# Optimization experiments

Measured on AMD Instinct MI355X. Metric: run time of the kernel, lower is better.

The kernel has to match this reference:

```python
import jax, jax.numpy as jnp
import numpy as np

N_NODES = 50000
N_EDGES = 600000
N_GRAPHS = 256


def gcn_conv(x, W, b, src, dst, n):
    # PyG GCNConv: out = D^{-1/2} (A + I) D^{-1/2} X W + b
    h = x @ W  # [N, out]
    deg = jax.ops.segment_sum(jnp.ones((src.shape[0],), h.dtype), dst, num_segments=n) + 1.0  # self-loop
    dinv = jax.lax.rsqrt(deg)  # deg >= 1 so safe
    msgs = h[src] * (dinv[src] * dinv[dst])[:, None]  # [E, out]
    agg = jax.ops.segment_sum(msgs, dst, num_segments=n)
    agg = agg + h * (dinv * dinv)[:, None]  # self-loop contribution
    return agg + b


def setup_inputs() -> dict:
    key = jax.random.key(0)
    ks = jax.random.split(key, 8)
    x = jax.random.normal(ks[0], (N_NODES, 1), dtype=jnp.float32)
    edge_index = jax.random.randint(ks[1], (2, N_EDGES), 0, N_NODES, dtype=jnp.int64)
    batch = jnp.sort(jax.random.randint(ks[2], (N_NODES,), 0, N_GRAPHS, dtype=jnp.int64))

    def glorot(k, shape):
        lim = np.sqrt(6.0 / (shape[0] + shape[1]))
        return jax.random.uniform(k, shape, jnp.float32, -lim, lim)

    return {
        "x": x,
        "W1": glorot(ks[3], (1, 64)), "b1": jnp.zeros((64,), jnp.float32),
        "W2": glorot(ks[4], (64, 128)), "b2": jnp.zeros((128,), jnp.float32),
        "W3": glorot(ks[5], (128, 64)), "b3": jnp.zeros((64,), jnp.float32),
        "lin1_w": glorot(ks[6], (64, 32)), "lin1_b": jnp.zeros((32,), jnp.float32),
        "lin2_w": glorot(ks[7], (32, 1)), "lin2_b": jnp.zeros((1,), jnp.float32),
        "edge_index": edge_index,
        "batch": batch,
    }


def reference(x, W1, b1, W2, b2, W3, b3, lin1_w, lin1_b, lin2_w, lin2_b, edge_index, batch):
    src, dst = edge_index[0], edge_index[1]
    n = x.shape[0]
    h = jax.nn.relu(gcn_conv(x, W1, b1, src, dst, n))
    h = jax.nn.relu(gcn_conv(h, W2, b2, src, dst, n))
    h = jax.nn.relu(gcn_conv(h, W3, b3, src, dst, n))
    # global_mean_pool
    sums = jax.ops.segment_sum(h, batch, num_segments=N_GRAPHS)
    cnts = jax.ops.segment_sum(jnp.ones((n,), h.dtype), batch, num_segments=N_GRAPHS)
    pooled = sums / jnp.maximum(cnts, 1.0)[:, None]  # [G, 64]
    z = jax.nn.relu(pooled @ lin1_w + lin1_b)
    return z @ lin2_w + lin2_b  # [G, 1]
```

## Files before the change

kernel.cpp:

```cpp
#include <hip/hip_runtime.h>


#define N_FEAT 64
#define POOL_SUB 16
#define SLOT 64

__global__ void fill_kernel(const int* __restrict__ src, const int* __restrict__ dst,
                            int* __restrict__ deg, int* __restrict__ csr, int E) {
    int e2 = (blockIdx.x * blockDim.x + threadIdx.x) * 2;
    if (e2 + 1 < E) {
        int2 sv = *(const int2*)&src[e2];
        int2 dv = *(const int2*)&dst[e2];
        int p0 = atomicAdd(&deg[dv.x], 1);
        int p1 = atomicAdd(&deg[dv.y], 1);
        csr[dv.x * SLOT + p0] = sv.x;
        csr[dv.y * SLOT + p1] = sv.y;
    } else if (e2 < E) {
        int d = dst[e2];
        int pos = atomicAdd(&deg[d], 1);
        csr[d * SLOT + pos] = src[e2];
    }
}

__global__ void prep_kernel(const int* __restrict__ deg, const float* __restrict__ x,
                            float* __restrict__ dinv, float* __restrict__ xd, int N) {
    int i = blockIdx.x * blockDim.x + threadIdx.x;
    if (i < N) {
        float dv = rsqrtf((float)deg[i] + 1.0f);
        dinv[i] = dv;
        xd[i] = x[i] * dv;
    }
}

__global__ void sagg_gather(const int* __restrict__ deg, const int* __restrict__ csr,
                            const float* __restrict__ xd, const float* __restrict__ dinv,
                            float2* __restrict__ sd, int N) {
    int wid = (blockIdx.x * blockDim.x + threadIdx.x) >> 6;
    int lane = threadIdx.x & 63;
    int v = wid * 4 + (lane >> 4);
    int sub = lane & 15;
    if (v >= N) return;
    int dg = deg[v];
    int base = v * SLOT;
    float sum = 0.0f;
    for (int j = sub; j < dg; j += 16) sum += xd[csr[base + j]];
    #pragma unroll
    for (int off = 8; off; off >>= 1) sum += __shfl_xor(sum, off);
    if (sub == 0) {
        float dv = dinv[v];
        sd[v] = make_float2(dv * (sum + xd[v]), dv);
    }
}

__global__ void agg1_gather(const int* __restrict__ deg, const int* __restrict__ csr,
                            const float2* __restrict__ sd,
                            const float* __restrict__ W1, const float* __restrict__ b1,
                            float* __restrict__ agg, int N) {
    int v = blockIdx.x * 4 + (threadIdx.x >> 6);
    int lane = threadIdx.x & 63;
    if (v >= N) return;
    float w1 = W1[lane], bb = b1[lane];
    int dg = deg[v];
    int base = v * SLOT;
    float acc = 0.0f;
    int j = 0;
    for (; j + 3 < dg; j += 4) {
        int u0 = csr[base + j], u1 = csr[base + j + 1];
        int u2 = csr[base + j + 2], u3 = csr[base + j + 3];
        float2 p0 = sd[u0];
        float2 p1 = sd[u1];
        float2 p2 = sd[u2];
        float2 p3 = sd[u3];
        acc += fmaxf(p0.x * w1 + bb, 0.0f) * p0.y + fmaxf(p1.x * w1 + bb, 0.0f) * p1.y;
        acc += fmaxf(p2.x * w1 + bb, 0.0f) * p2.y + fmaxf(p3.x * w1 + bb, 0.0f) * p3.y;
    }
    for (; j < dg; ++j) {
        float2 p = sd[csr[base + j]];
        acc += fmaxf(p.x * w1 + bb, 0.0f) * p.y;
    }
    float2 pv = sd[v];
    float dv = pv.y;
    agg[(size_t)v * N_FEAT + lane] = dv * acc + fmaxf(pv.x * w1 + bb, 0.0f) * dv * dv;
}

#define H2S 132
#define BM 32
__global__ __launch_bounds__(256) void gemm12(const float* __restrict__ A,
                                              const float* __restrict__ W2,
                                              const float* __restrict__ bias2,
                                              const float* __restrict__ W3,
                                              const float* __restrict__ dinv,
                                              float* __restrict__ md, int M) {
    __shared__ float Ws[128 * 64];
    __shared__ float Hs[BM * H2S];
    int tid = threadIdx.x;
    int row0 = blockIdx.x * BM;

    for (int idx = tid; idx < 64 * 128; idx += 256) Ws[idx] = W2[idx];
    {
        int r = tid >> 3;
        int kk = (tid & 7) * 8;
        int grow = row0 + r;
        float4 v0 = make_float4(0.f, 0.f, 0.f, 0.f), v1 = v0;
        if (grow < M) {
            v0 = *(const float4*)&A[(size_t)grow * 64 + kk];
            v1 = *(const float4*)&A[(size_t)grow * 64 + kk + 4];
        }
        *(float4*)&Hs[r * 64 + kk] = v0;
        *(float4*)&Hs[r * 64 + kk + 4] = v1;
    }
    __syncthreads();

    int c = (tid & 31) * 4;
    int rb = (tid >> 5) * 4;
    float acc1[4][4] = {};
    #pragma unroll 4
    for (int k = 0; k < 64; ++k) {
        float4 b = *(const float4*)&Ws[k * 128 + c];
        #pragma unroll
        for (int i = 0; i < 4; ++i) {
            float a = Hs[(rb + i) * 64 + k];
            acc1[i][0] += a * b.x; acc1[i][1] += a * b.y;
            acc1[i][2] += a * b.z; acc1[i][3] += a * b.w;
        }
    }
    float4 bv = *(const float4*)&bias2[c];
    __syncthreads();

    #pragma unroll
    for (int i = 0; i < 4; ++i) {
        float4 o;
        o.x = fmaxf(acc1[i][0] + bv.x, 0.f);
        o.y = fmaxf(acc1[i][1] + bv.y, 0.f);
        o.z = fmaxf(acc1[i][2] + bv.z, 0.f);
        o.w = fmaxf(acc1[i][3] + bv.w, 0.f);
        *(float4*)&Hs[(rb + i) * H2S + c] = o;
    }
    for (int idx = tid; idx < 128 * 64; idx += 256) Ws[idx] = W3[idx];
    __syncthreads();

    int c2 = (tid & 15) * 4;
    int r2 = (tid >> 4) * 2;
    float acc2[2][4] = {};
    for (int k0 = 0; k0 < 128; k0 += 4) {
        float4 w0 = *(const float4*)&Ws[(k0 + 0) * 64 + c2];
        float4 w1 = *(const float4*)&Ws[(k0 + 1) * 64 + c2];
        float4 w2 = *(const float4*)&Ws[(k0 + 2) * 64 + c2];
        float4 w3 = *(const float4*)&Ws[(k0 + 3) * 64 + c2];
        #pragma unroll
        for (int i = 0; i < 2; ++i) {
            float4 a = *(const float4*)&Hs[(r2 + i) * H2S + k0];
            acc2[i][0] += a.x * w0.x + a.y * w1.x + a.z * w2.x + a.w * w3.x;
            acc2[i][1] += a.x * w0.y + a.y * w1.y + a.z * w2.y + a.w * w3.y;
            acc2[i][2] += a.x * w0.z + a.y * w1.z + a.z * w2.z + a.w * w3.z;
            acc2[i][3] += a.x * w0.w + a.y * w1.w + a.z * w2.w + a.w * w3.w;
        }
    }
    #pragma unroll
    for (int i = 0; i < 2; ++i) {
        int grow = row0 + r2 + i;
        if (grow < M) {
            float dv = dinv[grow];
            float4 o = make_float4(acc2[i][0] * dv, acc2[i][1] * dv,
                                   acc2[i][2] * dv, acc2[i][3] * dv);
            *(float4*)&md[(size_t)grow * 64 + c2] = o;
        }
    }
}

__global__ void agg3_gather(const int* __restrict__ deg, const int* __restrict__ csr,
                            const float* __restrict__ md, const float* __restrict__ dinv,
                            float* __restrict__ agg, int N) {
    int v = blockIdx.x * 4 + (threadIdx.x >> 6);
    int lane = threadIdx.x & 63;
    if (v >= N) return;
    int dg = deg[v];
    int base = v * SLOT;
    float acc = md[(size_t)v * N_FEAT + lane];
    int j = 0;
    for (; j + 7 < dg; j += 8) {
        int u0 = csr[base + j],     u1 = csr[base + j + 1];
        int u2 = csr[base + j + 2], u3 = csr[base + j + 3];
        int u4 = csr[base + j + 4], u5 = csr[base + j + 5];
        int u6 = csr[base + j + 6], u7 = csr[base + j + 7];
        float a0 = md[(size_t)u0 * N_FEAT + lane];
        float a1 = md[(size_t)u1 * N_FEAT + lane];
        float a2 = md[(size_t)u2 * N_FEAT + lane];
        float a3 = md[(size_t)u3 * N_FEAT + lane];
        float a4 = md[(size_t)u4 * N_FEAT + lane];
        float a5 = md[(size_t)u5 * N_FEAT + lane];
        float a6 = md[(size_t)u6 * N_FEAT + lane];
        float a7 = md[(size_t)u7 * N_FEAT + lane];
        acc += ((a0 + a1) + (a2 + a3)) + ((a4 + a5) + (a6 + a7));
    }
    for (; j < dg; ++j) acc += md[(size_t)csr[base + j] * N_FEAT + lane];
    agg[(size_t)v * N_FEAT + lane] = acc * dinv[v];
}

__global__ void pool_kernel(const float* __restrict__ agg, const float* __restrict__ b3,
                            const int* __restrict__ batch, float* __restrict__ pooled,
                            float* __restrict__ counts, int N) {
    int wave = (blockIdx.x * blockDim.x + threadIdx.x) >> 6;
    int lane = threadIdx.x & 63;
    int start = wave * POOL_SUB;
    if (start >= N) return;
    int end = min(start + POOL_SUB, N);
    float bl = b3[lane];
    int cur = batch[start];
    float acc = 0.0f;
    float cnt = 0.0f;
    for (int i = start; i < end; ++i) {
        int g = batch[i];
        if (g != cur) {
            atomicAdd(&pooled[cur * N_FEAT + lane], acc);
            if (lane == 0) atomicAdd(&counts[cur], cnt);
            acc = 0.0f; cnt = 0.0f; cur = g;
        }
        acc += fmaxf(agg[(size_t)i * N_FEAT + lane] + bl, 0.0f);
        cnt += 1.0f;
    }
    atomicAdd(&pooled[cur * N_FEAT + lane], acc);
    if (lane == 0) atomicAdd(&counts[cur], cnt);
}

__global__ void mlp_kernel(const float* __restrict__ pooled, const float* __restrict__ counts,
                           const float* __restrict__ l1w, const float* __restrict__ l1b,
                           const float* __restrict__ l2w, const float* __restrict__ l2b,
                           float* __restrict__ out) {
    __shared__ float row[64];
    __shared__ float zs[32];
    int g = blockIdx.x;
    int l = threadIdx.x;
    float cnt = fmaxf(counts[g], 1.0f);
    row[l] = pooled[g * 64 + l] / cnt;
    __syncthreads();
    if (l < 32) {
        float z = l1b[l];
        #pragma unroll
        for (int k = 0; k < 64; ++k) z += row[k] * l1w[k * 32 + l];
        zs[l] = fmaxf(z, 0.0f);
    }
    __syncthreads();
    if (l == 0) {
        float o = l2b[0];
        #pragma unroll
        for (int j = 0; j < 32; ++j) o += zs[j] * l2w[j];
        out[g] = o;
    }
}

extern "C" void kernel_launch(void* const* d_in, const int* in_sizes, int n_in,
                              void* d_out, int out_size, void* d_ws, size_t ws_size,
                              hipStream_t stream) {
    const float* x   = (const float*)d_in[0];
    const float* W1  = (const float*)d_in[1];
    const float* b1  = (const float*)d_in[2];
    const float* W2  = (const float*)d_in[3];
    const float* b2  = (const float*)d_in[4];
    const float* W3  = (const float*)d_in[5];
    const float* b3  = (const float*)d_in[6];
    const float* l1w = (const float*)d_in[7];
    const float* l1b = (const float*)d_in[8];
    const float* l2w = (const float*)d_in[9];
    const float* l2b = (const float*)d_in[10];
    const int* ei    = (const int*)d_in[11];
    const int* batch = (const int*)d_in[12];

    int N = in_sizes[0];
    int E = in_sizes[11] / 2;
    int G = out_size;
    const int* src = ei;
    const int* dst = ei + E;

    char* wsb = (char*)d_ws;
    int*   deg      = (int*)wsb;                 wsb += (size_t)N * 4;
    float* pooled   = (float*)wsb;               wsb += (size_t)G * 64 * 4;
    float* counts   = (float*)wsb;               wsb += (size_t)G * 4;
    int*   csr      = (int*)wsb;                 wsb += (size_t)N * SLOT * 4;
    float* dinv     = (float*)wsb;               wsb += (size_t)N * 4;
    float* xd       = (float*)wsb;               wsb += (size_t)N * 4;
    float2* sd      = (float2*)wsb;              wsb += (size_t)N * 8;
    float* agg      = (float*)wsb;               wsb += (size_t)N * 64 * 4;
    float* md       = (float*)wsb;               wsb += (size_t)N * 64 * 4;

    hipMemsetAsync(deg, 0, ((size_t)N + (size_t)G * 64 + G) * 4, stream);

    int tb = 256;
    fill_kernel<<<(E / 2 + tb - 1) / tb, tb, 0, stream>>>(src, dst, deg, csr, E);
    prep_kernel<<<(N + tb - 1) / tb, tb, 0, stream>>>(deg, x, dinv, xd, N);
    sagg_gather<<<((N + 3) / 4 + 3) / 4, tb, 0, stream>>>(deg, csr, xd, dinv, sd, N);
    agg1_gather<<<(N + 3) / 4, tb, 0, stream>>>(deg, csr, sd, W1, b1, agg, N);
    gemm12<<<(N + BM - 1) / BM, tb, 0, stream>>>(agg, W2, b2, W3, dinv, md, N);
    agg3_gather<<<(N + 3) / 4, tb, 0, stream>>>(deg, csr, md, dinv, agg, N);
    int pool_waves = (N + POOL_SUB - 1) / POOL_SUB;
    pool_kernel<<<(pool_waves + 3) / 4, tb, 0, stream>>>(agg, b3, batch, pooled, counts, N);
    mlp_kernel<<<G, 64, 0, stream>>>(pooled, counts, l1w, l1b, l2w, l2b, (float*)d_out);
}
```

Baseline: 236.1 us.

## Widen fill loads, scalarize gather indices, vectorize gemm A-tile reads

The fill kernel now has each thread handle four edges with int4 loads instead of two, halving the thread count and issuing four atomics per thread. The agg1 and agg3 gathers route the node id and degree through readfirstlane so the compiler can treat them as wave-uniform scalars and issue CSR index loads as scalar loads. The first gemm loop reads four k values of the shared A tile at once with float4 and preloads four W rows per iteration, which cuts LDS instructions but uses more registers. The fill tail now loops in one thread, which is harmless because E is a multiple of four.

```diff
diff --git a/kernel.cpp b/kernel.cpp
--- a/kernel.cpp
+++ b/kernel.cpp
@@ -7,18 +7,24 @@
 
 __global__ void fill_kernel(const int* __restrict__ src, const int* __restrict__ dst,
                             int* __restrict__ deg, int* __restrict__ csr, int E) {
-    int e2 = (blockIdx.x * blockDim.x + threadIdx.x) * 2;
-    if (e2 + 1 < E) {
-        int2 sv = *(const int2*)&src[e2];
-        int2 dv = *(const int2*)&dst[e2];
+    int e4 = (blockIdx.x * blockDim.x + threadIdx.x) * 4;
+    if (e4 + 3 < E) {
+        int4 sv = *(const int4*)&src[e4];
+        int4 dv = *(const int4*)&dst[e4];
         int p0 = atomicAdd(&deg[dv.x], 1);
         int p1 = atomicAdd(&deg[dv.y], 1);
+        int p2 = atomicAdd(&deg[dv.z], 1);
+        int p3 = atomicAdd(&deg[dv.w], 1);
         csr[dv.x * SLOT + p0] = sv.x;
         csr[dv.y * SLOT + p1] = sv.y;
-    } else if (e2 < E) {
-        int d = dst[e2];
-        int pos = atomicAdd(&deg[d], 1);
-        csr[d * SLOT + pos] = src[e2];
+        csr[dv.z * SLOT + p2] = sv.z;
+        csr[dv.w * SLOT + p3] = sv.w;
+    } else {
+        for (int e = e4; e < E; ++e) {
+            int d = dst[e];
+            int pos = atomicAdd(&deg[d], 1);
+            csr[d * SLOT + pos] = src[e];
+        }
     }
 }
 
@@ -56,11 +62,11 @@
                             const float2* __restrict__ sd,
                             const float* __restrict__ W1, const float* __restrict__ b1,
                             float* __restrict__ agg, int N) {
-    int v = blockIdx.x * 4 + (threadIdx.x >> 6);
+    int v = __builtin_amdgcn_readfirstlane(blockIdx.x * 4 + (threadIdx.x >> 6));
     int lane = threadIdx.x & 63;
     if (v >= N) return;
     float w1 = W1[lane], bb = b1[lane];
-    int dg = deg[v];
+    int dg = __builtin_amdgcn_readfirstlane(deg[v]);
     int base = v * SLOT;
     float acc = 0.0f;
     int j = 0;
@@ -114,14 +120,18 @@
     int c = (tid & 31) * 4;
     int rb = (tid >> 5) * 4;
     float acc1[4][4] = {};
-    #pragma unroll 4
-    for (int k = 0; k < 64; ++k) {
-        float4 b = *(const float4*)&Ws[k * 128 + c];
+    for (int k0 = 0; k0 < 64; k0 += 4) {
+        float4 b0 = *(const float4*)&Ws[(k0 + 0) * 128 + c];
+        float4 b1v = *(const float4*)&Ws[(k0 + 1) * 128 + c];
+        float4 b2v = *(const float4*)&Ws[(k0 + 2) * 128 + c];
+        float4 b3v = *(const float4*)&Ws[(k0 + 3) * 128 + c];
         #pragma unroll
         for (int i = 0; i < 4; ++i) {
-            float a = Hs[(rb + i) * 64 + k];
-            acc1[i][0] += a * b.x; acc1[i][1] += a * b.y;
-            acc1[i][2] += a * b.z; acc1[i][3] += a * b.w;
+            float4 a = *(const float4*)&Hs[(rb + i) * 64 + k0];
+            acc1[i][0] += a.x * b0.x + a.y * b1v.x + a.z * b2v.x + a.w * b3v.x;
+            acc1[i][1] += a.x * b0.y + a.y * b1v.y + a.z * b2v.y + a.w * b3v.y;
+            acc1[i][2] += a.x * b0.z + a.y * b1v.z + a.z * b2v.z + a.w * b3v.z;
+            acc1[i][3] += a.x * b0.w + a.y * b1v.w + a.z * b2v.w + a.w * b3v.w;
         }
     }
     float4 bv = *(const float4*)&bias2[c];
@@ -171,10 +181,10 @@
 __global__ void agg3_gather(const int* __restrict__ deg, const int* __restrict__ csr,
                             const float* __restrict__ md, const float* __restrict__ dinv,
                             float* __restrict__ agg, int N) {
-    int v = blockIdx.x * 4 + (threadIdx.x >> 6);
+    int v = __builtin_amdgcn_readfirstlane(blockIdx.x * 4 + (threadIdx.x >> 6));
     int lane = threadIdx.x & 63;
     if (v >= N) return;
-    int dg = deg[v];
+    int dg = __builtin_amdgcn_readfirstlane(deg[v]);
     int base = v * SLOT;
     float acc = md[(size_t)v * N_FEAT + lane];
     int j = 0;
@@ -286,7 +296,7 @@
     hipMemsetAsync(deg, 0, ((size_t)N + (size_t)G * 64 + G) * 4, stream);
 
     int tb = 256;
-    fill_kernel<<<(E / 2 + tb - 1) / tb, tb, 0, stream>>>(src, dst, deg, csr, E);
+    fill_kernel<<<(E / 4 + tb - 1) / tb, tb, 0, stream>>>(src, dst, deg, csr, E);
     prep_kernel<<<(N + tb - 1) / tb, tb, 0, stream>>>(deg, x, dinv, xd, N);
     sagg_gather<<<((N + 3) / 4 + 3) / 4, tb, 0, stream>>>(deg, csr, xd, dinv, sd, N);
     agg1_gather<<<(N + 3) / 4, tb, 0, stream>>>(deg, csr, sd, W1, b1, agg, N);
```

Measured after the change: 225.1 us. -4.7%, faster.
